# Performance work log

Measured on AMD Instinct MI355X. Metric: run time of the kernel, lower is better.

## Reference

```python
import jax, jax.numpy as jnp
import numpy as np

EMB = 512
HEADS = 8
HD = EMB // HEADS
DEPTH = 6
CONT = 100
CAT_DIMS = [100] * 28
CAT = len(CAT_DIMS)
HID = int(EMB * (4.0 / 3.0))  # 682, FT-Transformer ReGLU hidden
B = 128
OFFSETS = jnp.asarray(np.concatenate([[0], np.cumsum(CAT_DIMS[:-1])]).astype(np.int32))
SQRT_EMB = float(np.sqrt(EMB))  # scores are DIVIDED by emb**-0.5 in the source


def setup_inputs() -> dict:
    key = jax.random.key(0)
    ks = jax.random.split(key, 16)
    s = 0.02
    x_cat = jax.random.randint(ks[0], (B, CAT), 0, CAT_DIMS[0]).astype(jnp.float32)
    x_cont = jax.random.normal(ks[1], (B, CONT), dtype=jnp.float32)
    x = jnp.concatenate([x_cat, x_cont], axis=1)  # [B, CAT+CONT]
    return {
        "x": x,
        "tok_w": jax.random.normal(ks[2], (CONT + 1, EMB)) * s,
        "tok_b": jax.random.normal(ks[3], (CONT + CAT, EMB)) * s,
        "cat_emb": jax.random.normal(ks[4], (sum(CAT_DIMS), EMB)) * s,
        "Wqkv": jax.random.normal(ks[5], (DEPTH, EMB, 3 * EMB)) * s,
        "bqkv": jnp.zeros((DEPTH, 3 * EMB)),
        "Wout": jax.random.normal(ks[6], (DEPTH, EMB, EMB)) * s,
        "bout": jnp.zeros((DEPTH, EMB)),
        "W0": jax.random.normal(ks[7], (DEPTH, EMB, 2 * HID)) * s,
        "b0": jnp.zeros((DEPTH, 2 * HID)),
        "W1": jax.random.normal(ks[8], (DEPTH, HID, EMB)) * s,
        "b1": jnp.zeros((DEPTH, EMB)),
        "ln0_g": jnp.ones((DEPTH, EMB)),
        "ln0_b": jnp.zeros((DEPTH, EMB)),
        "ln1_g": jnp.ones((DEPTH, EMB)),
        "ln1_b": jnp.zeros((DEPTH, EMB)),
    }


def _ln(x, g, b):
    m = x.mean(-1, keepdims=True)
    v = x.var(-1, keepdims=True)
    return (x - m) / jnp.sqrt(v + 1e-5) * g + b


def _attn(x, Wqkv, bqkv, Wout, bout):
    Bn, S, _ = x.shape
    # faithful layout: reshape to (B,S,H,3*hd), move heads, chunk last dim
    qkv = (x @ Wqkv + bqkv).reshape(Bn, S, HEADS, 3 * HD).transpose(0, 2, 1, 3)
    q, k, v = jnp.split(qkv, 3, axis=-1)  # each [B,H,S,hd]
    scores = jnp.einsum("bhqd,bhkd->bhqk", q, k) * SQRT_EMB  # / (emb**-0.5)
    attn = jax.nn.softmax(jax.nn.softmax(scores, axis=-1), axis=-1)  # double softmax, as in source
    o = jnp.einsum("bhqk,bhkd->bhqd", attn, v)
    o = o.transpose(0, 2, 1, 3).reshape(Bn, S, EMB)
    return o @ Wout + bout


def _reglu(x):
    a, b = jnp.split(x, 2, axis=-1)
    return a * jax.nn.relu(b)


def _forward(x, tok_w, tok_b, cat_emb, Wqkv, bqkv, Wout, bout, W0, b0, W1, b1,
             ln0_g, ln0_b, ln1_g, ln1_b):
    # --- feature tokenizer ---
    x_cats = x[:, :CAT].astype(jnp.int32)
    x_conts = jnp.concatenate([jnp.ones((x.shape[0], 1), x.dtype), x[:, CAT:]], axis=1)  # [B, CONT+1]
    h = tok_w[None] * x_conts[:, :, None]  # [B, CONT+1, EMB]
    h = jnp.concatenate([h, cat_emb[x_cats + OFFSETS[None]]], axis=1)  # [B, S=129, EMB]
    bias = jnp.concatenate([jnp.zeros((1, EMB), h.dtype), tok_b], axis=0)
    h = h + bias[None]
    # --- transformer stack ---
    for i in range(DEPTH):
        xin = _ln(h, ln0_g[i], ln0_b[i]) if i else h  # layer 0 has no norm0
        h = h + _attn(xin, Wqkv[i], bqkv[i], Wout[i], bout[i])
        r = _ln(h, ln1_g[i], ln1_b[i])
        r = _reglu(r @ W0[i] + b0[i]) @ W1[i] + b1[i]
        h = h + r
    return h[:, 0]  # CLS token


def reference(x, tok_w, tok_b, cat_emb, Wqkv, bqkv, Wout, bout, W0, b0, W1, b1,
              ln0_g, ln0_b, ln1_g, ln1_b):
    return _forward(x, tok_w, tok_b, cat_emb, Wqkv, bqkv, Wout, bout, W0, b0, W1, b1,
                    ln0_g, ln0_b, ln1_g, ln1_b)
```

## Files before the change

### kernel.cpp

```cpp
#include <hip/hip_runtime.h>
#include <hip/hip_bf16.h>
#include <stdint.h>


typedef __hip_bfloat16 bf16_t;
typedef __attribute__((ext_vector_type(8))) __bf16 bf16x8;
typedef __attribute__((ext_vector_type(4))) float floatx4;

#define AS1 __attribute__((address_space(1)))
#define AS3 __attribute__((address_space(3)))

constexpr int M_ROWS = 16512;
constexpr float SQRT_EMB_F = 22.627416997969522f;

__device__ __forceinline__ void gload_lds16(const void* g, void* l) {
  __builtin_amdgcn_global_load_lds((const AS1 unsigned int*)g, (AS3 unsigned int*)l, 16, 0, 0);
}

__device__ __forceinline__ floatx4 mfma16(bf16x8 a, bf16x8 b, floatx4 c) {
  return __builtin_amdgcn_mfma_f32_16x16x32_bf16(a, b, c, 0, 0, 0);
}

template <int PERM>
__global__ __launch_bounds__(256) void transpose_cvt(const float* __restrict__ W,
    bf16_t* __restrict__ WT, int K, int N, int KP, int NP)
{
  __shared__ float tile[32][33];
  int k0 = blockIdx.x * 32, n0 = blockIdx.y * 32;
  const float* Wl = W + (size_t)blockIdx.z * K * N;
  bf16_t* WTl = WT + (size_t)blockIdx.z * NP * KP;
  #pragma unroll
  for (int r = 0; r < 32; r += 8) {
    int k = k0 + threadIdx.y + r, n = n0 + threadIdx.x;
    int srcn = PERM ? ((n & 1) ? 682 + (n >> 1) : (n >> 1)) : n;
    int valid = (k < K) && (PERM ? (n < 1364) : (n < N));
    tile[threadIdx.y + r][threadIdx.x] = valid ? Wl[(size_t)k * N + srcn] : 0.f;
  }
  __syncthreads();
  #pragma unroll
  for (int r = 0; r < 32; r += 8) {
    int n = n0 + threadIdx.y + r, k = k0 + threadIdx.x;
    if (n < NP && k < KP)
      WTl[(size_t)n * KP + k] = __float2bfloat16(tile[threadIdx.x][threadIdx.y + r]);
  }
}

__global__ __launch_bounds__(256) void tokenizer_kernel(const float* __restrict__ x,
    const float* __restrict__ tok_w, const float* __restrict__ tok_b,
    const float* __restrict__ cat_emb, float* __restrict__ h, bf16_t* __restrict__ ab)
{
  int row = blockIdx.x;
  int b = row / 129, t = row - b * 129;
  float* hr = h + (size_t)row * 512;
  bf16_t* ar = ab + (size_t)row * 512;
  for (int e = threadIdx.x; e < 512; e += 256) {
    float val;
    if (t == 0) {
      val = tok_w[e];
    } else if (t <= 100) {
      val = tok_w[(size_t)t * 512 + e] * x[(size_t)b * 128 + 28 + (t - 1)]
            + tok_b[(size_t)(t - 1) * 512 + e];
    } else {
      int j = t - 101;
      int idx = (int)x[(size_t)b * 128 + j] + 100 * j;
      val = cat_emb[(size_t)idx * 512 + e] + tok_b[(size_t)(t - 1) * 512 + e];
    }
    hr[e] = val;
    ar[e] = __float2bfloat16(val);
  }
}

__global__ __launch_bounds__(256) void ln_kernel(const float* __restrict__ hin,
    bf16_t* __restrict__ out, const float* __restrict__ g, const float* __restrict__ bta)
{
  int row = blockIdx.x * 4 + (threadIdx.x >> 6);
  int lane = threadIdx.x & 63;
  const float* hr = hin + (size_t)row * 512 + lane * 8;
  float4 v0 = *(const float4*)hr;
  float4 v1 = *(const float4*)(hr + 4);
  float s = v0.x + v0.y + v0.z + v0.w + v1.x + v1.y + v1.z + v1.w;
  float q = v0.x * v0.x + v0.y * v0.y + v0.z * v0.z + v0.w * v0.w
          + v1.x * v1.x + v1.y * v1.y + v1.z * v1.z + v1.w * v1.w;
  #pragma unroll
  for (int o = 1; o < 64; o <<= 1) { s += __shfl_xor(s, o); q += __shfl_xor(q, o); }
  float mean = s * (1.f / 512.f);
  float var = q * (1.f / 512.f) - mean * mean;
  float rstd = rsqrtf(var + 1e-5f);
  float4 g0 = *(const float4*)(g + lane * 8);
  float4 g1 = *(const float4*)(g + lane * 8 + 4);
  float4 b0v = *(const float4*)(bta + lane * 8);
  float4 b1v = *(const float4*)(bta + lane * 8 + 4);
  bf16x8 o8;
  o8[0] = (__bf16)__float2bfloat16((v0.x - mean) * rstd * g0.x + b0v.x);
  o8[1] = (__bf16)__float2bfloat16((v0.y - mean) * rstd * g0.y + b0v.y);
  o8[2] = (__bf16)__float2bfloat16((v0.z - mean) * rstd * g0.z + b0v.z);
  o8[3] = (__bf16)__float2bfloat16((v0.w - mean) * rstd * g0.w + b0v.w);
  o8[4] = (__bf16)__float2bfloat16((v1.x - mean) * rstd * g1.x + b1v.x);
  o8[5] = (__bf16)__float2bfloat16((v1.y - mean) * rstd * g1.y + b1v.y);
  o8[6] = (__bf16)__float2bfloat16((v1.z - mean) * rstd * g1.z + b1v.z);
  o8[7] = (__bf16)__float2bfloat16((v1.w - mean) * rstd * g1.w + b1v.w);
  *(bf16x8*)(out + (size_t)row * 512 + lane * 8) = o8;
}

template <int MODE>
__global__ __launch_bounds__(256) void gemm_bt(const bf16_t* __restrict__ A,
    const bf16_t* __restrict__ BT, const float* __restrict__ bias, int biasN,
    const float* __restrict__ resid, void* __restrict__ outp, int K, int N)
{
  __shared__ bf16_t As[128 * 32];
  __shared__ bf16_t Bs[128 * 32];
  const int total = gridDim.x * gridDim.y;
  const int lin = blockIdx.y * gridDim.x + blockIdx.x;
  const int xcd = lin & 7, kb = lin >> 3;
  const int qch = total >> 3, rch = total & 7;
  const int idx = xcd * qch + (xcd < rch ? xcd : rch) + kb;
  const int bm = idx / gridDim.x;
  const int bn = idx - bm * gridDim.x;
  const int m0 = bm * 128, n0 = bn * 128;

  const int tid = threadIdx.x;
  const int w = tid >> 6, l = tid & 63, l15 = l & 15, quad = l >> 4;
  const int wm = (w >> 1) * 64, wn = (w & 1) * 64;
  const bf16_t* Ab = A + (size_t)m0 * K;
  const bf16_t* Bb = BT + (size_t)n0 * K;
  const int r0 = tid >> 2;
  const int kc0 = (((tid & 3) ^ ((tid >> 3) & 3))) * 8;
  const int swz = (l15 >> 1) & 3;

  floatx4 z4 = {0.f, 0.f, 0.f, 0.f};
  floatx4 acc[4][4];
  #pragma unroll
  for (int i = 0; i < 4; i++)
    #pragma unroll
    for (int j = 0; j < 4; j++) acc[i][j] = z4;

  for (int kk = 0; kk < K; kk += 32) {
    gload_lds16(Ab + (size_t)r0 * K + kk + kc0,        &As[tid * 8]);
    gload_lds16(Ab + (size_t)(r0 + 64) * K + kk + kc0, &As[(tid + 256) * 8]);
    gload_lds16(Bb + (size_t)r0 * K + kk + kc0,        &Bs[tid * 8]);
    gload_lds16(Bb + (size_t)(r0 + 64) * K + kk + kc0, &Bs[(tid + 256) * 8]);
    __syncthreads();
    bf16x8 af[4], bfr[4];
    #pragma unroll
    for (int i = 0; i < 4; i++) {
      af[i]  = *(const bf16x8*)&As[(wm + i * 16 + l15) * 32 + ((quad ^ swz) * 8)];
      bfr[i] = *(const bf16x8*)&Bs[(wn + i * 16 + l15) * 32 + ((quad ^ swz) * 8)];
    }
    #pragma unroll
    for (int i = 0; i < 4; i++)
      #pragma unroll
      for (int j = 0; j < 4; j++)
        acc[i][j] = mfma16(af[i], bfr[j], acc[i][j]);
    __syncthreads();
  }

  #pragma unroll
  for (int j = 0; j < 4; j++) {
    int col = n0 + wn + j * 16 + l15;
    float bv = 0.f;
    if (MODE == 2) {
      if (col < biasN) bv = bias[(col & 1) ? 682 + (col >> 1) : (col >> 1)];
    } else {
      if (col < biasN) bv = bias[col];
    }
    #pragma unroll
    for (int i = 0; i < 4; i++) {
      int row_b = m0 + wm + i * 16 + quad * 4;
      #pragma unroll
      for (int r = 0; r < 4; r++) {
        float v = acc[i][j][r] + bv;
        if (MODE == 2) {
          float other = __shfl_xor(v, 1);
          if (!(l15 & 1)) {
            size_t idx2 = (size_t)(row_b + r) * (N >> 1) + (col >> 1);
            ((bf16_t*)outp)[idx2] = __float2bfloat16(v * fmaxf(other, 0.f));
          }
        } else {
          size_t idx2 = (size_t)(row_b + r) * N + col;
          if (MODE == 1) ((float*)outp)[idx2] = v + resid[idx2];
          else           ((bf16_t*)outp)[idx2] = __float2bfloat16(v);
        }
      }
    }
  }
}

constexpr int SP = 160;
__global__ __launch_bounds__(256) void attn_kernel(const bf16_t* __restrict__ qkv,
                                                   bf16_t* __restrict__ attnout)
{
  __shared__ bf16_t vt_lds[64 * SP];
  __shared__ float sc[32 * SP];
  bf16_t* p_lds = (bf16_t*)sc;

  const int bh = blockIdx.x, b = bh >> 3, hh = bh & 7;
  const int tid = threadIdx.x;
  const int w = tid >> 6, l = tid & 63, l15 = l & 15, quad = l >> 4;
  const bf16_t* base = qkv + (size_t)b * 129 * 1536 + hh * 192;

  for (int i = tid; i < SP * 64 / 2; i += 256) ((unsigned int*)vt_lds)[i] = 0u;
  __syncthreads();
  for (int c = tid; c < 129 * 8; c += 256) {
    int s = c >> 3, ch = c & 7;
    float4 tmp4 = *(const float4*)(base + (size_t)s * 1536 + 128 + ch * 8);
    const bf16_t* tv = (const bf16_t*)&tmp4;
    #pragma unroll
    for (int j = 0; j < 8; j++) vt_lds[(size_t)(ch * 8 + j) * SP + s] = tv[j];
  }
  __syncthreads();

  for (int qt = 0; qt < 5; qt++) {
    bf16x8 zq = {};
    bf16x8 aq[2][2];
    #pragma unroll
    for (int mt = 0; mt < 2; mt++) {
      int m = qt * 32 + mt * 16 + l15;
      #pragma unroll
      for (int t = 0; t < 2; t++)
        aq[mt][t] = (m < 129) ? *(const bf16x8*)(base + (size_t)m * 1536 + t * 32 + quad * 8) : zq;
    }
    for (int nt = w; nt < 10; nt += 4) {
      int krow = nt * 16 + l15;
      floatx4 a0 = {0.f, 0.f, 0.f, 0.f}, a1 = {0.f, 0.f, 0.f, 0.f};
      #pragma unroll
      for (int t = 0; t < 2; t++) {
        bf16x8 kf = (krow < 129)
            ? *(const bf16x8*)(base + (size_t)krow * 1536 + 64 + t * 32 + quad * 8) : zq;
        a0 = mfma16(aq[0][t], kf, a0);
        a1 = mfma16(aq[1][t], kf, a1);
      }
      #pragma unroll
      for (int r = 0; r < 4; r++) {
        sc[(quad * 4 + r) * SP + nt * 16 + l15]      = a0[r] * SQRT_EMB_F;
        sc[(16 + quad * 4 + r) * SP + nt * 16 + l15] = a1[r] * SQRT_EMB_F;
      }
    }
    __syncthreads();

    {
      int row = tid >> 3, sub = tid & 7;
      float vv[20];
      float mx = -1e30f;
      #pragma unroll
      for (int c = 0; c < 20; c++) {
        int j = sub + c * 8;
        vv[c] = (j < 129) ? sc[row * SP + j] : -1e30f;
        mx = fmaxf(mx, vv[c]);
      }
      #pragma unroll
      for (int o = 1; o < 8; o <<= 1) mx = fmaxf(mx, __shfl_xor(mx, o, 8));
      float sum = 0.f;
      #pragma unroll
      for (int c = 0; c < 20; c++) {
        int j = sub + c * 8;
        vv[c] = (j < 129) ? __expf(vv[c] - mx) : 0.f;
        sum += vv[c];
      }
      #pragma unroll
      for (int o = 1; o < 8; o <<= 1) sum += __shfl_xor(sum, o, 8);
      float inv = 1.f / sum;
      float mx2 = 0.f;
      #pragma unroll
      for (int c = 0; c < 20; c++) { vv[c] *= inv; mx2 = fmaxf(mx2, vv[c]); }
      #pragma unroll
      for (int o = 1; o < 8; o <<= 1) mx2 = fmaxf(mx2, __shfl_xor(mx2, o, 8));
      float sum2 = 0.f;
      #pragma unroll
      for (int c = 0; c < 20; c++) {
        int j = sub + c * 8;
        vv[c] = (j < 129) ? __expf(vv[c] - mx2) : 0.f;
        sum2 += vv[c];
      }
      #pragma unroll
      for (int o = 1; o < 8; o <<= 1) sum2 += __shfl_xor(sum2, o, 8);
      float inv2 = 1.f / sum2;
      __syncthreads();
      #pragma unroll
      for (int c = 0; c < 20; c++) {
        int j = sub + c * 8;
        p_lds[row * SP + j] = __float2bfloat16(vv[c] * inv2);
      }
    }
    __syncthreads();

    {
      int mt = w >> 1, nt0 = (w & 1) * 2;
      floatx4 oacc[2];
      oacc[0] = floatx4{0.f, 0.f, 0.f, 0.f};
      oacc[1] = floatx4{0.f, 0.f, 0.f, 0.f};
      #pragma unroll
      for (int t = 0; t < 5; t++) {
        bf16x8 pf = *(const bf16x8*)&p_lds[(mt * 16 + l15) * SP + t * 32 + quad * 8];
        #pragma unroll
        for (int n = 0; n < 2; n++) {
          bf16x8 vf = *(const bf16x8*)&vt_lds[((nt0 + n) * 16 + l15) * SP + t * 32 + quad * 8];
          oacc[n] = mfma16(pf, vf, oacc[n]);
        }
      }
      #pragma unroll
      for (int n = 0; n < 2; n++)
        #pragma unroll
        for (int r = 0; r < 4; r++) {
          int sq = qt * 32 + mt * 16 + quad * 4 + r;
          if (sq < 129)
            attnout[((size_t)b * 129 + sq) * 512 + hh * 64 + (nt0 + n) * 16 + l15] =
                __float2bfloat16(oacc[n][r]);
        }
    }
    __syncthreads();
  }
}

__global__ __launch_bounds__(256) void out_copy(const float* __restrict__ h,
                                                float* __restrict__ out)
{
  int b = blockIdx.x, e = threadIdx.x;
  out[(size_t)b * 512 + e]       = h[(size_t)b * 129 * 512 + e];
  out[(size_t)b * 512 + e + 256] = h[(size_t)b * 129 * 512 + e + 256];
}

extern "C" void kernel_launch(void* const* d_in, const int* in_sizes, int n_in,
                              void* d_out, int out_size, void* d_ws, size_t ws_size,
                              hipStream_t stream)
{
  const float* x       = (const float*)d_in[0];
  const float* tok_w   = (const float*)d_in[1];
  const float* tok_b   = (const float*)d_in[2];
  const float* cat_emb = (const float*)d_in[3];
  const float* Wqkv    = (const float*)d_in[4];
  const float* bqkv    = (const float*)d_in[5];
  const float* Wout    = (const float*)d_in[6];
  const float* bout    = (const float*)d_in[7];
  const float* W0      = (const float*)d_in[8];
  const float* b0      = (const float*)d_in[9];
  const float* W1      = (const float*)d_in[10];
  const float* b1      = (const float*)d_in[11];
  const float* ln0_g   = (const float*)d_in[12];
  const float* ln0_b   = (const float*)d_in[13];
  const float* ln1_g   = (const float*)d_in[14];
  const float* ln1_b   = (const float*)d_in[15];

  size_t off = 0;
  char* base = (char*)d_ws;
  auto alloc = [&](size_t n) { char* p = base + off; off += (n + 255) & ~(size_t)255; return p; };
  float*  h     = (float*) alloc((size_t)M_ROWS * 512 * 4);
  bf16_t* ab    = (bf16_t*)alloc((size_t)M_ROWS * 512 * 2);
  bf16_t* qkv   = (bf16_t*)alloc((size_t)M_ROWS * 1536 * 2);
  bf16_t* attno = (bf16_t*)alloc((size_t)M_ROWS * 512 * 2);
  bf16_t* regl  = (bf16_t*)alloc((size_t)M_ROWS * 704 * 2);
  bf16_t* WqkvT = (bf16_t*)alloc((size_t)6 * 1536 * 512 * 2);
  bf16_t* WoutT = (bf16_t*)alloc((size_t)6 * 512 * 512 * 2);
  bf16_t* W0T   = (bf16_t*)alloc((size_t)6 * 1408 * 512 * 2);
  bf16_t* W1T   = (bf16_t*)alloc((size_t)6 * 512 * 704 * 2);
  (void)ws_size; (void)in_sizes; (void)n_in; (void)out_size;

  dim3 tb(32, 8, 1);
  transpose_cvt<0><<<dim3(16, 48, 6), tb, 0, stream>>>(Wqkv, WqkvT, 512, 1536, 512, 1536);
  transpose_cvt<0><<<dim3(16, 16, 6), tb, 0, stream>>>(Wout, WoutT, 512, 512, 512, 512);
  transpose_cvt<1><<<dim3(16, 44, 6), tb, 0, stream>>>(W0, W0T, 512, 1364, 512, 1408);
  transpose_cvt<0><<<dim3(22, 16, 6), tb, 0, stream>>>(W1, W1T, 682, 512, 704, 512);

  tokenizer_kernel<<<M_ROWS, 256, 0, stream>>>(x, tok_w, tok_b, cat_emb, h, ab);

  for (int i = 0; i < 6; i++) {
    if (i)
      ln_kernel<<<M_ROWS / 4, 256, 0, stream>>>(h, ab, ln0_g + (size_t)i * 512,
                                                ln0_b + (size_t)i * 512);
    gemm_bt<0><<<dim3(12, 129), 256, 0, stream>>>(
        ab, WqkvT + (size_t)i * 1536 * 512, bqkv + (size_t)i * 1536, 1536, nullptr, qkv, 512, 1536);
    attn_kernel<<<1024, 256, 0, stream>>>(qkv, attno);
    gemm_bt<1><<<dim3(4, 129), 256, 0, stream>>>(
        attno, WoutT + (size_t)i * 512 * 512, bout + (size_t)i * 512, 512, h, h, 512, 512);
    ln_kernel<<<M_ROWS / 4, 256, 0, stream>>>(h, ab, ln1_g + (size_t)i * 512,
                                              ln1_b + (size_t)i * 512);
    gemm_bt<2><<<dim3(11, 129), 256, 0, stream>>>(
        ab, W0T + (size_t)i * 1408 * 512, b0 + (size_t)i * 1364, 1364, nullptr, regl, 512, 1408);
    gemm_bt<1><<<dim3(4, 129), 256, 0, stream>>>(
        regl, W1T + (size_t)i * 512 * 704, b1 + (size_t)i * 512, 512, h, h, 704, 512);
  }

  out_copy<<<128, 256, 0, stream>>>(h, (float*)d_out);
}
```

Measured before the change: 1.509 ms.

## Triple-buffer GEMM LDS tiles with async global-to-LDS prefetch two stages ahead

The bf16 MFMA GEMM now keeps three LDS buffers for the A and B tiles and issues global_load_lds for tile t+2 while it computes tile t. It replaces the two __syncthreads per iteration with a manual vmcnt wait and a single s_barrier. The aim is to hide global-memory latency behind the MFMA work instead of stalling on each K step. The cost is three times the LDS use (48KB per block), which may lower occupancy, and the hand-coded waitcnt values must correctly cover the outstanding loads.

```diff
diff --git a/kernel.cpp b/kernel.cpp
--- a/kernel.cpp
+++ b/kernel.cpp
@@ -19,6 +19,12 @@
 
 __device__ __forceinline__ floatx4 mfma16(bf16x8 a, bf16x8 b, floatx4 c) {
   return __builtin_amdgcn_mfma_f32_16x16x32_bf16(a, b, c, 0, 0, 0);
+}
+
+__device__ __forceinline__ void block_barrier() {
+  asm volatile("" ::: "memory");
+  __builtin_amdgcn_s_barrier();
+  asm volatile("" ::: "memory");
 }
 
 template <int PERM>
@@ -107,8 +113,8 @@
     const bf16_t* __restrict__ BT, const float* __restrict__ bias, int biasN,
     const float* __restrict__ resid, void* __restrict__ outp, int K, int N)
 {
-  __shared__ bf16_t As[128 * 32];
-  __shared__ bf16_t Bs[128 * 32];
+  __shared__ bf16_t As[3][128 * 32];
+  __shared__ bf16_t Bs[3][128 * 32];
   const int total = gridDim.x * gridDim.y;
   const int lin = blockIdx.y * gridDim.x + blockIdx.x;
   const int xcd = lin & 7, kb = lin >> 3;
@@ -126,6 +132,16 @@
   const int r0 = tid >> 2;
   const int kc0 = (((tid & 3) ^ ((tid >> 3) & 3))) * 8;
   const int swz = (l15 >> 1) & 3;
+  const size_t a0o = (size_t)r0 * K + kc0;
+  const size_t a1o = (size_t)(r0 + 64) * K + kc0;
+
+  auto issue = [&](int t, int buf) {
+    const int kk = t * 32;
+    gload_lds16(Ab + a0o + kk, &As[buf][tid * 8]);
+    gload_lds16(Ab + a1o + kk, &As[buf][(tid + 256) * 8]);
+    gload_lds16(Bb + a0o + kk, &Bs[buf][tid * 8]);
+    gload_lds16(Bb + a1o + kk, &Bs[buf][(tid + 256) * 8]);
+  };
 
   floatx4 z4 = {0.f, 0.f, 0.f, 0.f};
   floatx4 acc[4][4];
@@ -134,24 +150,30 @@
     #pragma unroll
     for (int j = 0; j < 4; j++) acc[i][j] = z4;
 
-  for (int kk = 0; kk < K; kk += 32) {
-    gload_lds16(Ab + (size_t)r0 * K + kk + kc0,        &As[tid * 8]);
-    gload_lds16(Ab + (size_t)(r0 + 64) * K + kk + kc0, &As[(tid + 256) * 8]);
-    gload_lds16(Bb + (size_t)r0 * K + kk + kc0,        &Bs[tid * 8]);
-    gload_lds16(Bb + (size_t)(r0 + 64) * K + kk + kc0, &Bs[(tid + 256) * 8]);
-    __syncthreads();
+  const int T = K >> 5;
+  issue(0, 0);
+  issue(1, 1);
+  int cur = 0, nxt2 = 2;
+  for (int t = 0; t < T; t++) {
+    if (t + 1 < T) __builtin_amdgcn_s_waitcnt(0x0F74);
+    else           __builtin_amdgcn_s_waitcnt(0x0F70);
+    block_barrier();
+    if (t + 2 < T) issue(t + 2, nxt2);
+    const bf16_t* Ac = As[cur];
+    const bf16_t* Bc = Bs[cur];
     bf16x8 af[4], bfr[4];
     #pragma unroll
     for (int i = 0; i < 4; i++) {
-      af[i]  = *(const bf16x8*)&As[(wm + i * 16 + l15) * 32 + ((quad ^ swz) * 8)];
-      bfr[i] = *(const bf16x8*)&Bs[(wn + i * 16 + l15) * 32 + ((quad ^ swz) * 8)];
+      af[i]  = *(const bf16x8*)&Ac[(wm + i * 16 + l15) * 32 + ((quad ^ swz) * 8)];
+      bfr[i] = *(const bf16x8*)&Bc[(wn + i * 16 + l15) * 32 + ((quad ^ swz) * 8)];
     }
     #pragma unroll
     for (int i = 0; i < 4; i++)
       #pragma unroll
       for (int j = 0; j < 4; j++)
         acc[i][j] = mfma16(af[i], bfr[j], acc[i][j]);
-    __syncthreads();
+    cur = (cur == 2) ? 0 : cur + 1;
+    nxt2 = (nxt2 == 2) ? 0 : nxt2 + 1;
   }
 
   #pragma unroll
```

Result: faster. 1.412 ms (-6.4%).

## Store GEMM operands in MFMA fragment-major layout and load directly to registers

Applied to the files above, without the earlier changes.

All bf16 activations and transposed weights are written in a fragment-tiled layout (16-row by 32-k chunks of 512 elements), so every lane can fetch its MFMA operand with one contiguous 16-byte global load. The GEMM drops LDS staging and barriers and uses register double-buffering of fragments, with launch bounds raised to allow three blocks per CU. The producers (tokenizer, layernorm, attention output, ReGLU epilogue) and the attention loads are rewritten for the new layout. The cost is that data reuse across waves now relies on L1/L2 instead of LDS, and the extra register pressure may cause spills.

```diff
diff --git a/kernel.cpp b/kernel.cpp
--- a/kernel.cpp
+++ b/kernel.cpp
@@ -7,18 +7,18 @@
 typedef __attribute__((ext_vector_type(8))) __bf16 bf16x8;
 typedef __attribute__((ext_vector_type(4))) float floatx4;
 
-#define AS1 __attribute__((address_space(1)))
-#define AS3 __attribute__((address_space(3)))
-
 constexpr int M_ROWS = 16512;
 constexpr float SQRT_EMB_F = 22.627416997969522f;
 
-__device__ __forceinline__ void gload_lds16(const void* g, void* l) {
-  __builtin_amdgcn_global_load_lds((const AS1 unsigned int*)g, (AS3 unsigned int*)l, 16, 0, 0);
-}
-
 __device__ __forceinline__ floatx4 mfma16(bf16x8 a, bf16x8 b, floatx4 c) {
   return __builtin_amdgcn_mfma_f32_16x16x32_bf16(a, b, c, 0, 0, 0);
+}
+
+__device__ __forceinline__ size_t frag_chunk(int m, int k, int KT) {
+  return ((size_t)(m >> 4) * KT + (k >> 5)) * 512 + (m & 15) * 8 + 128 * ((k >> 3) & 3);
+}
+__device__ __forceinline__ size_t frag_elem(int m, int k, int KT) {
+  return frag_chunk(m, k, KT) + (k & 7);
 }
 
 template <int PERM>
@@ -29,6 +29,7 @@
   int k0 = blockIdx.x * 32, n0 = blockIdx.y * 32;
   const float* Wl = W + (size_t)blockIdx.z * K * N;
   bf16_t* WTl = WT + (size_t)blockIdx.z * NP * KP;
+  const int KT = KP >> 5;
   #pragma unroll
   for (int r = 0; r < 32; r += 8) {
     int k = k0 + threadIdx.y + r, n = n0 + threadIdx.x;
@@ -41,7 +42,7 @@
   for (int r = 0; r < 32; r += 8) {
     int n = n0 + threadIdx.y + r, k = k0 + threadIdx.x;
     if (n < NP && k < KP)
-      WTl[(size_t)n * KP + k] = __float2bfloat16(tile[threadIdx.x][threadIdx.y + r]);
+      WTl[frag_elem(n, k, KT)] = __float2bfloat16(tile[threadIdx.x][threadIdx.y + r]);
   }
 }
 
@@ -49,25 +50,34 @@
     const float* __restrict__ tok_w, const float* __restrict__ tok_b,
     const float* __restrict__ cat_emb, float* __restrict__ h, bf16_t* __restrict__ ab)
 {
-  int row = blockIdx.x;
+  int row = blockIdx.x * 4 + (threadIdx.x >> 6);
+  int lane = threadIdx.x & 63, e0 = lane * 8;
   int b = row / 129, t = row - b * 129;
-  float* hr = h + (size_t)row * 512;
-  bf16_t* ar = ab + (size_t)row * 512;
-  for (int e = threadIdx.x; e < 512; e += 256) {
-    float val;
-    if (t == 0) {
-      val = tok_w[e];
-    } else if (t <= 100) {
-      val = tok_w[(size_t)t * 512 + e] * x[(size_t)b * 128 + 28 + (t - 1)]
-            + tok_b[(size_t)(t - 1) * 512 + e];
-    } else {
-      int j = t - 101;
-      int idx = (int)x[(size_t)b * 128 + j] + 100 * j;
-      val = cat_emb[(size_t)idx * 512 + e] + tok_b[(size_t)(t - 1) * 512 + e];
-    }
-    hr[e] = val;
-    ar[e] = __float2bfloat16(val);
-  }
+  float v[8];
+  if (t == 0) {
+    #pragma unroll
+    for (int u = 0; u < 8; u++) v[u] = tok_w[e0 + u];
+  } else if (t <= 100) {
+    float xv = x[(size_t)b * 128 + 28 + (t - 1)];
+    const float* wp = tok_w + (size_t)t * 512 + e0;
+    const float* bp = tok_b + (size_t)(t - 1) * 512 + e0;
+    #pragma unroll
+    for (int u = 0; u < 8; u++) v[u] = wp[u] * xv + bp[u];
+  } else {
+    int j = t - 101;
+    int idx = (int)x[(size_t)b * 128 + j] + 100 * j;
+    const float* cp = cat_emb + (size_t)idx * 512 + e0;
+    const float* bp = tok_b + (size_t)(t - 1) * 512 + e0;
+    #pragma unroll
+    for (int u = 0; u < 8; u++) v[u] = cp[u] + bp[u];
+  }
+  float* hr = h + (size_t)row * 512 + e0;
+  #pragma unroll
+  for (int u = 0; u < 8; u++) hr[u] = v[u];
+  bf16x8 o8;
+  #pragma unroll
+  for (int u = 0; u < 8; u++) o8[u] = (__bf16)__float2bfloat16(v[u]);
+  *(bf16x8*)(ab + ((size_t)(row >> 4) * 16 + (lane >> 2)) * 512 + (row & 15) * 8 + 128 * (lane & 3)) = o8;
 }
 
 __global__ __launch_bounds__(256) void ln_kernel(const float* __restrict__ hin,
@@ -99,21 +109,19 @@
   o8[5] = (__bf16)__float2bfloat16((v1.y - mean) * rstd * g1.y + b1v.y);
   o8[6] = (__bf16)__float2bfloat16((v1.z - mean) * rstd * g1.z + b1v.z);
   o8[7] = (__bf16)__float2bfloat16((v1.w - mean) * rstd * g1.w + b1v.w);
-  *(bf16x8*)(out + (size_t)row * 512 + lane * 8) = o8;
+  *(bf16x8*)(out + ((size_t)(row >> 4) * 16 + (lane >> 2)) * 512 + (row & 15) * 8 + 128 * (lane & 3)) = o8;
 }
 
 template <int MODE>
-__global__ __launch_bounds__(256) void gemm_bt(const bf16_t* __restrict__ A,
+__global__ __launch_bounds__(256, 3) void gemm_frag(const bf16_t* __restrict__ A,
     const bf16_t* __restrict__ BT, const float* __restrict__ bias, int biasN,
     const float* __restrict__ resid, void* __restrict__ outp, int K, int N)
 {
-  __shared__ bf16_t As[128 * 32];
-  __shared__ bf16_t Bs[128 * 32];
   const int total = gridDim.x * gridDim.y;
   const int lin = blockIdx.y * gridDim.x + blockIdx.x;
-  const int xcd = lin & 7, kb = lin >> 3;
+  const int xcd = lin & 7, kb2 = lin >> 3;
   const int qch = total >> 3, rch = total & 7;
-  const int idx = xcd * qch + (xcd < rch ? xcd : rch) + kb;
+  const int idx = xcd * qch + (xcd < rch ? xcd : rch) + kb2;
   const int bm = idx / gridDim.x;
   const int bn = idx - bm * gridDim.x;
   const int m0 = bm * 128, n0 = bn * 128;
@@ -121,11 +129,22 @@
   const int tid = threadIdx.x;
   const int w = tid >> 6, l = tid & 63, l15 = l & 15, quad = l >> 4;
   const int wm = (w >> 1) * 64, wn = (w & 1) * 64;
-  const bf16_t* Ab = A + (size_t)m0 * K;
-  const bf16_t* Bb = BT + (size_t)n0 * K;
-  const int r0 = tid >> 2;
-  const int kc0 = (((tid & 3) ^ ((tid >> 3) & 3))) * 8;
-  const int swz = (l15 >> 1) & 3;
+  const int KT = K >> 5;
+
+  const bf16_t* pa[4];
+  const bf16_t* pb[4];
+  #pragma unroll
+  for (int i = 0; i < 4; i++) {
+    pa[i] = A  + ((size_t)(((m0 + wm) >> 4) + i) * KT) * 512 + l * 8;
+    pb[i] = BT + ((size_t)(((n0 + wn) >> 4) + i) * KT) * 512 + l * 8;
+  }
+
+  bf16x8 af[2][4], bg[2][4];
+  #pragma unroll
+  for (int i = 0; i < 4; i++) {
+    af[0][i] = *(const bf16x8*)pa[i];
+    bg[0][i] = *(const bf16x8*)pb[i];
+  }
 
   floatx4 z4 = {0.f, 0.f, 0.f, 0.f};
   floatx4 acc[4][4];
@@ -134,24 +153,34 @@
     #pragma unroll
     for (int j = 0; j < 4; j++) acc[i][j] = z4;
 
-  for (int kk = 0; kk < K; kk += 32) {
-    gload_lds16(Ab + (size_t)r0 * K + kk + kc0,        &As[tid * 8]);
-    gload_lds16(Ab + (size_t)(r0 + 64) * K + kk + kc0, &As[(tid + 256) * 8]);
-    gload_lds16(Bb + (size_t)r0 * K + kk + kc0,        &Bs[tid * 8]);
-    gload_lds16(Bb + (size_t)(r0 + 64) * K + kk + kc0, &Bs[(tid + 256) * 8]);
-    __syncthreads();
-    bf16x8 af[4], bfr[4];
-    #pragma unroll
-    for (int i = 0; i < 4; i++) {
-      af[i]  = *(const bf16x8*)&As[(wm + i * 16 + l15) * 32 + ((quad ^ swz) * 8)];
-      bfr[i] = *(const bf16x8*)&Bs[(wn + i * 16 + l15) * 32 + ((quad ^ swz) * 8)];
+  const int T = KT;
+  for (int t = 0; t < T; t += 2) {
+    if (t + 1 < T) {
+      #pragma unroll
+      for (int i = 0; i < 4; i++) {
+        af[1][i] = *(const bf16x8*)(pa[i] + (size_t)(t + 1) * 512);
+        bg[1][i] = *(const bf16x8*)(pb[i] + (size_t)(t + 1) * 512);
+      }
     }
     #pragma unroll
     for (int i = 0; i < 4; i++)
       #pragma unroll
       for (int j = 0; j < 4; j++)
-        acc[i][j] = mfma16(af[i], bfr[j], acc[i][j]);
-    __syncthreads();
+        acc[i][j] = mfma16(af[0][i], bg[0][j], acc[i][j]);
+    if (t + 1 < T) {
+      if (t + 2 < T) {
+        #pragma unroll
+        for (int i = 0; i < 4; i++) {
+          af[0][i] = *(const bf16x8*)(pa[i] + (size_t)(t + 2) * 512);
+          bg[0][i] = *(const bf16x8*)(pb[i] + (size_t)(t + 2) * 512);
+        }
+      }
+      #pragma unroll
+      for (int i = 0; i < 4; i++)
+        #pragma unroll
+        for (int j = 0; j < 4; j++)
+          acc[i][j] = mfma16(af[1][i], bg[1][j], acc[i][j]);
+    }
   }
 
   #pragma unroll
@@ -169,16 +198,19 @@
       #pragma unroll
       for (int r = 0; r < 4; r++) {
         float v = acc[i][j][r] + bv;
+        int m = row_b + r;
         if (MODE == 2) {
           float other = __shfl_xor(v, 1);
           if (!(l15 & 1)) {
-            size_t idx2 = (size_t)(row_b + r) * (N >> 1) + (col >> 1);
-            ((bf16_t*)outp)[idx2] = __float2bfloat16(v * fmaxf(other, 0.f));
+            int c2 = col >> 1;
+            ((bf16_t*)outp)[frag_elem(m, c2, (N >> 1) >> 5)] =
+                __float2bfloat16(v * fmaxf(other, 0.f));
           }
+        } else if (MODE == 1) {
+          size_t idx2 = (size_t)m * N + col;
+          ((float*)outp)[idx2] = v + resid[idx2];
         } else {
-          size_t idx2 = (size_t)(row_b + r) * N + col;
-          if (MODE == 1) ((float*)outp)[idx2] = v + resid[idx2];
-          else           ((bf16_t*)outp)[idx2] = __float2bfloat16(v);
+          ((bf16_t*)outp)[frag_elem(m, col, N >> 5)] = __float2bfloat16(v);
         }
       }
     }
@@ -192,20 +224,20 @@
   __shared__ bf16_t vt_lds[64 * SP];
   __shared__ float sc[32 * SP];
   bf16_t* p_lds = (bf16_t*)sc;
+  __bf16* vt_raw = (__bf16*)vt_lds;
 
   const int bh = blockIdx.x, b = bh >> 3, hh = bh & 7;
   const int tid = threadIdx.x;
   const int w = tid >> 6, l = tid & 63, l15 = l & 15, quad = l >> 4;
-  const bf16_t* base = qkv + (size_t)b * 129 * 1536 + hh * 192;
+  const int rbase = b * 129;
 
   for (int i = tid; i < SP * 64 / 2; i += 256) ((unsigned int*)vt_lds)[i] = 0u;
   __syncthreads();
   for (int c = tid; c < 129 * 8; c += 256) {
     int s = c >> 3, ch = c & 7;
-    float4 tmp4 = *(const float4*)(base + (size_t)s * 1536 + 128 + ch * 8);
-    const bf16_t* tv = (const bf16_t*)&tmp4;
-    #pragma unroll
-    for (int j = 0; j < 8; j++) vt_lds[(size_t)(ch * 8 + j) * SP + s] = tv[j];
+    bf16x8 tv = *(const bf16x8*)(qkv + frag_chunk(rbase + s, hh * 192 + 128 + ch * 8, 48));
+    #pragma unroll
+    for (int j = 0; j < 8; j++) vt_raw[(size_t)(ch * 8 + j) * SP + s] = tv[j];
   }
   __syncthreads();
 
@@ -217,7 +249,8 @@
       int m = qt * 32 + mt * 16 + l15;
       #pragma unroll
       for (int t = 0; t < 2; t++)
-        aq[mt][t] = (m < 129) ? *(const bf16x8*)(base + (size_t)m * 1536 + t * 32 + quad * 8) : zq;
+        aq[mt][t] = (m < 129)
+            ? *(const bf16x8*)(qkv + frag_chunk(rbase + m, hh * 192 + t * 32 + quad * 8, 48)) : zq;
     }
     for (int nt = w; nt < 10; nt += 4) {
       int krow = nt * 16 + l15;
@@ -225,7 +258,8 @@
       #pragma unroll
       for (int t = 0; t < 2; t++) {
         bf16x8 kf = (krow < 129)
-            ? *(const bf16x8*)(base + (size_t)krow * 1536 + 64 + t * 32 + quad * 8) : zq;
+            ? *(const bf16x8*)(qkv + frag_chunk(rbase + krow, hh * 192 + 64 + t * 32 + quad * 8, 48))
+            : zq;
         a0 = mfma16(aq[0][t], kf, a0);
         a1 = mfma16(aq[1][t], kf, a1);
       }
@@ -302,9 +336,10 @@
         #pragma unroll
         for (int r = 0; r < 4; r++) {
           int sq = qt * 32 + mt * 16 + quad * 4 + r;
-          if (sq < 129)
-            attnout[((size_t)b * 129 + sq) * 512 + hh * 64 + (nt0 + n) * 16 + l15] =
-                __float2bfloat16(oacc[n][r]);
+          if (sq < 129) {
+            int cc = hh * 64 + (nt0 + n) * 16 + l15;
+            attnout[frag_elem(rbase + sq, cc, 16)] = __float2bfloat16(oacc[n][r]);
+          }
         }
     }
     __syncthreads();
@@ -360,22 +395,22 @@
   transpose_cvt<1><<<dim3(16, 44, 6), tb, 0, stream>>>(W0, W0T, 512, 1364, 512, 1408);
   transpose_cvt<0><<<dim3(22, 16, 6), tb, 0, stream>>>(W1, W1T, 682, 512, 704, 512);
 
-  tokenizer_kernel<<<M_ROWS, 256, 0, stream>>>(x, tok_w, tok_b, cat_emb, h, ab);
+  tokenizer_kernel<<<M_ROWS / 4, 256, 0, stream>>>(x, tok_w, tok_b, cat_emb, h, ab);
 
   for (int i = 0; i < 6; i++) {
     if (i)
       ln_kernel<<<M_ROWS / 4, 256, 0, stream>>>(h, ab, ln0_g + (size_t)i * 512,
                                                 ln0_b + (size_t)i * 512);
-    gemm_bt<0><<<dim3(12, 129), 256, 0, stream>>>(
+    gemm_frag<0><<<dim3(12, 129), 256, 0, stream>>>(
         ab, WqkvT + (size_t)i * 1536 * 512, bqkv + (size_t)i * 1536, 1536, nullptr, qkv, 512, 1536);
     attn_kernel<<<1024, 256, 0, stream>>>(qkv, attno);
-    gemm_bt<1><<<dim3(4, 129), 256, 0, stream>>>(
+    gemm_frag<1><<<dim3(4, 129), 256, 0, stream>>>(
         attno, WoutT + (size_t)i * 512 * 512, bout + (size_t)i * 512, 512, h, h, 512, 512);
     ln_kernel<<<M_ROWS / 4, 256, 0, stream>>>(h, ab, ln1_g + (size_t)i * 512,
                                               ln1_b + (size_t)i * 512);
-    gemm_bt<2><<<dim3(11, 129), 256, 0, stream>>>(
+    gemm_frag<2><<<dim3(11, 129), 256, 0, stream>>>(
         ab, W0T + (size_t)i * 1408 * 512, b0 + (size_t)i * 1364, 1364, nullptr, regl, 512, 1408);
-    gemm_bt<1><<<dim3(4, 129), 256, 0, stream>>>(
+    gemm_frag<1><<<dim3(4, 129), 256, 0, stream>>>(
         regl, W1T + (size_t)i * 512 * 704, b1 + (size_t)i * 512, 512, h, h, 704, 512);
   }
 
```

After: 1.273 ms. -15.6%, faster.
